# Kernel optimization log

Measured on AMD Instinct MI355X. Metric: run time of the kernel, lower is better.

The kernel has to match this reference:

```python
import jax, jax.numpy as jnp
import numpy as np

XBOUND = (-30.0, 30.0, 0.25)
YBOUND = (-15.0, 15.0, 0.25)
ZBOUND = (-1.0, 1.0, 0.5)
EPS = 1e-9


def _heights():
    n = int((ZBOUND[1] - ZBOUND[0]) // ZBOUND[2]) + 1
    return [ZBOUND[0] + i * ZBOUND[2] for i in range(n)]


def _bev_planes():
    # matches construct_plane_grid: linspace endpoints included, meshgrid(y, x) 'ij'
    num_x = int((XBOUND[1] - XBOUND[0]) / XBOUND[2])
    num_y = int((YBOUND[1] - YBOUND[0]) / YBOUND[2])
    x = jnp.linspace(XBOUND[0], XBOUND[1], num_x, dtype=jnp.float32)
    y = jnp.linspace(YBOUND[0], YBOUND[1], num_y, dtype=jnp.float32)
    yy, xx = jnp.meshgrid(y, x, indexing='ij')
    planes = [jnp.stack([xx, yy, jnp.full_like(xx, h)], axis=-1) for h in _heights()]
    return jnp.stack(planes)  # (nlvl, bH, bW, 3)


def _bilinear_grid_sample(im, grid):
    # faithful port of the manual pad+floor+gather grid_sample (align_corners=False)
    n, c, h, w = im.shape
    gh, gw = grid.shape[1], grid.shape[2]
    x = ((grid[..., 0] + 1) * w - 1) / 2
    y = ((grid[..., 1] + 1) * h - 1) / 2
    x = x.reshape(n, -1)
    y = y.reshape(n, -1)
    x0 = jnp.floor(x)
    y0 = jnp.floor(y)
    wa = ((x0 + 1 - x) * (y0 + 1 - y))[:, None, :]
    wb = ((x0 + 1 - x) * (y - y0))[:, None, :]
    wc = ((x - x0) * (y0 + 1 - y))[:, None, :]
    wd = ((x - x0) * (y - y0))[:, None, :]
    pw, ph = w + 2, h + 2
    # clip in float first to avoid int32 overflow; out-of-range lands on zero padding either way
    x0f = jnp.clip(x0, -2.0, w + 2.0)
    y0f = jnp.clip(y0, -2.0, h + 2.0)
    x0i = jnp.clip(x0f.astype(jnp.int32) + 1, 0, pw - 1)
    x1i = jnp.clip(x0f.astype(jnp.int32) + 2, 0, pw - 1)
    y0i = jnp.clip(y0f.astype(jnp.int32) + 1, 0, ph - 1)
    y1i = jnp.clip(y0f.astype(jnp.int32) + 2, 0, ph - 1)
    im_flat = jnp.pad(im, ((0, 0), (0, 0), (1, 1), (1, 1))).reshape(n, c, -1)

    def gather(xi, yi):
        return jnp.take_along_axis(im_flat, (xi + yi * pw)[:, None, :], axis=2)

    out = (gather(x0i, y0i) * wa + gather(x0i, y1i) * wb
           + gather(x1i, y0i) * wc + gather(x1i, y1i) * wd)
    return out.reshape(n, c, gh, gw)


def _campos(pts, ego2cam, img_h, img_w):
    # pts: (B, q, 3); ego2cam: (B, ncam, 4, 4)
    B, q, _ = pts.shape
    ncam = ego2cam.shape[1]
    pts_h = jnp.concatenate([pts, jnp.ones_like(pts[..., :1])], axis=-1)  # (B,q,4)
    cam = jnp.einsum('bnij,bqj->bnqi', ego2cam, pts_h)  # (B,ncam,q,4)
    z = cam[..., 2:3]
    mask = z > EPS
    xy = cam[..., 0:2] / z + EPS
    px = xy[..., 0:1] / img_w
    py = xy[..., 1:2] / img_h
    p = (jnp.concatenate([px, py], axis=-1) - 0.5) * 2
    mask = (mask & (p[..., 0:1] > -1.0) & (p[..., 0:1] < 1.0)
            & (p[..., 1:2] > -1.0) & (p[..., 1:2] < 1.0))
    return p.reshape(B * ncam, q, 2), mask.reshape(B, ncam, q)


def reference(cam_feat, ego2cam, conv_w, conv_b, img_h, img_w):
    B, ncam = ego2cam.shape[0], ego2cam.shape[1]
    C = cam_feat.shape[1]
    planes = _bev_planes().astype(cam_feat.dtype)  # (nlvl,bH,bW,3)
    nlvl, bH, bW, _ = planes.shape
    pts = jnp.broadcast_to(planes.reshape(1, -1, 3), (B, nlvl * bH * bW, 3))
    pos, mask = _campos(pts, ego2cam, img_h, img_w)
    grid = pos.reshape(B * ncam, nlvl * bH, bW, 2)
    proj = _bilinear_grid_sample(cam_feat, grid).reshape(B, ncam, C, nlvl, bH, bW)
    m = mask.reshape(B, ncam, 1, nlvl, bH, bW).astype(proj.dtype)
    feat = (proj * m).sum(axis=1)            # (B,C,nlvl,bH,bW)
    num = m.sum(axis=1)                      # (B,1,nlvl,bH,bW)
    feat = feat / jnp.where(num == 0, jnp.ones_like(num), num)
    coords = jnp.broadcast_to(jnp.transpose(planes, (3, 0, 1, 2))[None], (B, 3, nlvl, bH, bW))
    feat = jnp.concatenate([feat, coords], axis=1).reshape(B, (C + 3) * nlvl, bH, bW)
    out = jax.lax.conv_general_dilated(
        feat, conv_w, window_strides=(1, 1), padding=((1, 1), (1, 1)),
        dimension_numbers=('NCHW', 'OIHW', 'NCHW'))
    return out + conv_b[None, :, None, None]


def setup_inputs() -> dict:
    key = jax.random.key(0)
    k1, k2, k3 = jax.random.split(key, 3)
    B, ncam, C = 1, 6, 128
    cH, cW = 64, 176
    nlvl = 5
    cam_feat = jax.random.normal(k1, (B * ncam, C, cH, cW), dtype=jnp.float32)
    ego2cam = jax.random.normal(k2, (B, ncam, 4, 4), dtype=jnp.float32)
    conv_w = jax.random.normal(k3, (128, (C + 3) * nlvl, 3, 3), dtype=jnp.float32) * 0.02
    conv_b = jnp.zeros((128,), dtype=jnp.float32)
    return {'cam_feat': cam_feat, 'ego2cam': ego2cam, 'conv_w': conv_w,
            'conv_b': conv_b, 'img_h': 512, 'img_w': 1408}
```

## Files before the change

### kernel.cpp

```cpp
#include <hip/hip_runtime.h>
#include <hip/hip_bf16.h>

#define BH 120
#define BW 240
#define NLVL 5
#define NCAM 6
#define CH 128
#define FH 64
#define FW 176
#define CIN 655
#define CINP 672
#define NCT 21
#define FROWS 124
#define FCOLS 242
#define NPIX (BH*BW)

typedef __hip_bfloat16 bf16;
typedef __attribute__((ext_vector_type(8))) short s16x8;
typedef __attribute__((ext_vector_type(4))) float f32x4;
typedef unsigned int uint;
typedef __attribute__((ext_vector_type(4), aligned(4))) uint uint4a;

#define G_AS __attribute__((address_space(1)))
#define L_AS __attribute__((address_space(3)))

__device__ __forceinline__ float bf2f(unsigned short u) {
    union { unsigned int i; float f; } c; c.i = ((unsigned int)u) << 16; return c.f;
}
__device__ __forceinline__ uint f2bu(float x) {
    return (uint)__hip_bfloat16_raw(__float2bfloat16(x)).x;
}
__device__ __forceinline__ float blo(uint u) {
    union { uint i; float f; } c; c.i = u << 16; return c.f;
}
__device__ __forceinline__ float bhi(uint u) {
    union { uint i; float f; } c; c.i = u & 0xFFFF0000u; return c.f;
}

__global__ __launch_bounds__(256) void transpose_kernel(
    const float* __restrict__ in, bf16* __restrict__ out)
{
    __shared__ float t[32][129];
    int n = blockIdx.z, h = blockIdx.y, w0 = blockIdx.x * 32;
    int wlim = min(32, FW - w0);
    int wx = threadIdx.x & 31, cg = threadIdx.x >> 5;
    if (wx < wlim) {
        #pragma unroll
        for (int k = 0; k < 16; ++k) {
            int c = cg + k * 8;
            t[wx][c] = in[((n*CH + c)*FH + h)*FW + w0 + wx];
        }
    }
    __syncthreads();
    int c2 = threadIdx.x & 127, wi = threadIdx.x >> 7;
    for (int w = wi; w < wlim; w += 2)
        out[((n*FH + h)*FW + w0 + w)*CH + c2] = __float2bfloat16(t[w][c2]);
}

__global__ __launch_bounds__(256) void wprep_kernel(
    const float* __restrict__ w, bf16* __restrict__ wbf)
{
    int idx = blockIdx.x * 256 + threadIdx.x;
    if (idx >= 128 * CINP) return;
    int oc = idx / CINP, cin = idx - oc * CINP;
    float v[9];
    if (cin < CIN) {
        const float* s = w + ((size_t)oc * CIN + cin) * 9;
        #pragma unroll
        for (int k = 0; k < 9; ++k) v[k] = s[k];
    } else {
        #pragma unroll
        for (int k = 0; k < 9; ++k) v[k] = 0.f;
    }
    #pragma unroll
    for (int k = 0; k < 9; ++k)
        wbf[(size_t)(k * 128 + oc) * CINP + cin] = __float2bfloat16(v[k]);
}

__global__ __launch_bounds__(128) void border_kernel(bf16* __restrict__ feat)
{
    int b = blockIdx.x;
    int row, col;
    if (b < 242)      { row = 0;   col = b; }
    else if (b < 484) { row = 121; col = b - 242; }
    else if (b < 604) { row = b - 484 + 1; col = 0; }
    else              { row = b - 604 + 1; col = 241; }
    s16x8* p = (s16x8*)(feat + ((size_t)row*FCOLS + col)*CINP);
    int t = threadIdx.x;
    if (t < 84) p[t] = (s16x8){0,0,0,0,0,0,0,0};
}

__global__ __launch_bounds__(256) void proj_kernel(
    const bf16* __restrict__ camt,
    const float* __restrict__ e2c,
    const int* __restrict__ pimgh, const int* __restrict__ pimgw,
    bf16* __restrict__ feat)
{
    __shared__ int   s_soff[4][32];
    __shared__ float s_w4[4][30][4];
    __shared__ int   s_val[4][32];

    const int wv = threadIdx.x >> 6;
    const int lane = threadIdx.x & 63;
    const int bid = blockIdx.x;
    const int swz = (bid & 7) * 900 + (bid >> 3);
    const int pix = swz * 4 + wv;
    const int bx = pix % BW, by = pix / BW;
    float xw = (float)(-30.0 + bx * (60.0/239.0)); if (bx == BW-1) xw = 30.f;
    float yw = (float)(-15.0 + by * (30.0/119.0)); if (by == BH-1) yw = 15.f;

    const bool act = lane < 30;
    int valid = 0, ix = 0, iy = 0, cam = 0;
    float fx = 0.f, fy = 0.f;
    if (act) {
        int l = lane / 6; cam = lane - l*6;
        float h = -1.f + 0.5f * (float)l;
        const float* M = e2c + cam * 16;
        float cx = M[0]*xw + M[1]*yw + M[2]*h  + M[3];
        float cy = M[4]*xw + M[5]*yw + M[6]*h  + M[7];
        float cz = M[8]*xw + M[9]*yw + M[10]*h + M[11];
        float iw = (float)pimgw[0], ih = (float)pimgh[0];
        float px = ((cx/cz + 1e-9f)/iw - 0.5f) * 2.f;
        float py = ((cy/cz + 1e-9f)/ih - 0.5f) * 2.f;
        valid = (cz > 1e-9f) && (px > -1.f) && (px < 1.f)
                             && (py > -1.f) && (py < 1.f);
        float xs = ((px + 1.f)*(float)FW - 1.f) * 0.5f;
        float ys = ((py + 1.f)*(float)FH - 1.f) * 0.5f;
        float x0 = floorf(xs), y0 = floorf(ys);
        fx = xs - x0; fy = ys - y0;
        ix = (int)x0; iy = (int)y0;
        s_val[wv][lane] = valid;
    }
    __syncthreads();
    if (act) {
        int lbase = (lane / 6) * 6;
        int cnt = s_val[wv][lbase] + s_val[wv][lbase+1] + s_val[wv][lbase+2]
                + s_val[wv][lbase+3] + s_val[wv][lbase+4] + s_val[wv][lbase+5];
        float inv = (cnt > 0) ? (1.f / (float)cnt) : 0.f;
        float sc = valid ? inv : 0.f;
        int bx0 = min(max(ix, 0), FW-2);
        int by0 = min(max(iy, 0), FH-2);
        float gx0 = (1.f - fx) * sc, gx1 = fx * sc;
        float wx0 = 0.f, wx1 = 0.f;
        if (ix >= 0)     { if (ix == bx0) wx0 += gx0; else wx1 += gx0; }
        if (ix+1 <= FW-1){ if (ix+1 == bx0) wx0 += gx1; else wx1 += gx1; }
        float wy0 = 0.f, wy1 = 0.f;
        float gy0 = 1.f - fy, gy1 = fy;
        if (iy >= 0)     { if (iy == by0) wy0 += gy0; else wy1 += gy0; }
        if (iy+1 <= FH-1){ if (iy+1 == by0) wy0 += gy1; else wy1 += gy1; }
        s_w4[wv][lane][0] = wx0 * wy0;
        s_w4[wv][lane][1] = wx0 * wy1;
        s_w4[wv][lane][2] = wx1 * wy0;
        s_w4[wv][lane][3] = wx1 * wy1;
        s_soff[wv][lane] = valid ? ((cam*FH + by0)*FW + bx0)*CH : -1;
    }
    __syncthreads();

    const int c2 = lane * 2;
    float va[NLVL], vb[NLVL];
    #pragma unroll
    for (int l = 0; l < NLVL; ++l) { va[l] = 0.f; vb[l] = 0.f; }

    #pragma unroll
    for (int l = 0; l < NLVL; ++l) {
        #pragma unroll
        for (int cm = 0; cm < NCAM; ++cm) {
            int id = l*6 + cm;
            int so = s_soff[wv][id];
            if (so >= 0) {
                const bf16* bp = camt + so + c2;
                uint q0 = *(const uint*)(bp);
                uint q2 = *(const uint*)(bp + CH);
                uint q1 = *(const uint*)(bp + FW*CH);
                uint q3 = *(const uint*)(bp + FW*CH + CH);
                float w0 = s_w4[wv][id][0], w1 = s_w4[wv][id][1];
                float w2 = s_w4[wv][id][2], w3 = s_w4[wv][id][3];
                va[l] += w0*blo(q0) + w1*blo(q1) + w2*blo(q2) + w3*blo(q3);
                vb[l] += w0*bhi(q0) + w1*bhi(q1) + w2*bhi(q2) + w3*bhi(q3);
            }
        }
    }

    bf16* dpix = feat + ((size_t)(by+1)*FCOLS + (bx+1))*CINP;
    uint u0 = f2bu(va[0]) | (f2bu(va[1]) << 16);
    uint u1 = f2bu(va[2]) | (f2bu(va[3]) << 16);
    uint u2 = f2bu(va[4]) | (f2bu(vb[0]) << 16);
    uint u3 = f2bu(vb[1]) | (f2bu(vb[2]) << 16);
    uint u4 = f2bu(vb[3]) | (f2bu(vb[4]) << 16);
    char* dst = (char*)(dpix + c2*5);
    *(uint4a*)dst = (uint4a){u0, u1, u2, u3};
    *(uint*)(dst + 16) = u4;
    if (lane < 15) {
        int j = lane / 5, l = lane - j*5;
        float v = (j == 0) ? xw : (j == 1) ? yw : (-1.f + 0.5f*(float)l);
        dpix[CH*5 + lane] = __float2bfloat16(v);
    }
}

__global__ __launch_bounds__(256, 2) void conv_mfma_kernel(
    const bf16* __restrict__ feat,
    const bf16* __restrict__ wbf,
    bf16* __restrict__ part)
{
    __shared__ __align__(16) char lds[61440];
    const int tid  = threadIdx.x;
    const int wv   = tid >> 6;
    const int lane = tid & 63;
    const int t15  = tid & 15;
    const int kgl  = (tid >> 4) & 3;
    const int y0p = blockIdx.y * 8;
    const int x0p = blockIdx.x * 32;
    const int q   = blockIdx.z;
    const int ct0 = q ? (1 + 5*q) : 0;
    const int nct = q ? 5 : 6;
    const int nph = nct * 9;

    const int HB0 = 0, HB1 = 22528, WB0 = 45056, WB1 = 53248;

    f32x4 acc[8][4];
    #pragma unroll
    for (int m = 0; m < 8; ++m)
        #pragma unroll
        for (int f = 0; f < 4; ++f)
            acc[m][f] = (f32x4){0.f, 0.f, 0.f, 0.f};

    auto stageW = [&](int ct, int off, int wb) {
        #pragma unroll
        for (int jj = 0; jj < 2; ++jj) {
            int j = 2*wv + jj;
            int cch = j*64 + lane;
            int oc = cch >> 2, kgp = cch & 3;
            int kg = kgp ^ ((oc >> 1) & 3);
            const bf16* src = wbf + ((size_t)(off*128 + oc)*CINP + ct*32 + kg*8);
            __builtin_amdgcn_global_load_lds((const G_AS void*)src,
                                             (L_AS void*)(lds + wb + j*1024),
                                             16, 0, 0);
        }
    };
    auto stageH = [&](int ct, int hb) {
        for (int j = wv; j < 22; j += 4) {
            int cch = j*64 + lane;
            int pp = cch >> 2, kgp = cch & 3;
            int kg = kgp ^ ((pp >> 1) & 3);
            int row = pp / 34;
            int col = pp - row*34;
            int gc = min(x0p + col, FCOLS-1);
            const bf16* src = feat + ((size_t)(y0p + row)*FCOLS + gc)*CINP
                                   + ct*32 + kg*8;
            __builtin_amdgcn_global_load_lds((const G_AS void*)src,
                                             (L_AS void*)(lds + hb + j*1024),
                                             16, 0, 0);
        }
    };

    stageH(ct0, HB0);
    stageW(ct0, 0, WB0);
    __syncthreads();

    int lct = 0, off = 0;
    for (int p = 0; p < nph; ++p) {
        if (p + 1 < nph) {
            int off1 = off + 1, lct1 = lct;
            if (off1 == 9) { off1 = 0; ++lct1; }
            stageW(ct0 + lct1, off1, ((p+1) & 1) ? WB1 : WB0);
            if (off1 == 0) stageH(ct0 + lct1, (lct1 & 1) ? HB1 : HB0);
        }
        const int wb = (p & 1) ? WB1 : WB0;
        const int hb = (lct & 1) ? HB1 : HB0;
        const int ky = off / 3, kx = off - ky*3;

        s16x8 A[8];
        #pragma unroll
        for (int m = 0; m < 8; ++m) {
            int oc = m*16 + t15;
            A[m] = *(const s16x8*)(lds + wb + oc*64 + ((kgl ^ ((oc>>1)&3)) << 4));
        }
        #pragma unroll
        for (int f = 0; f < 4; ++f) {
            const int fr = f >> 1, fc = f & 1;
            int hp = (2*wv + fr + ky)*34 + fc*16 + t15 + kx;
            s16x8 Bv = *(const s16x8*)(lds + hb + hp*64
                                       + ((kgl ^ ((hp>>1)&3)) << 4));
            __builtin_amdgcn_s_setprio(1);
            #pragma unroll
            for (int m = 0; m < 8; ++m)
                acc[m][f] = __builtin_amdgcn_mfma_f32_16x16x32_bf16(
                                A[m], Bv, acc[m][f], 0, 0, 0);
            __builtin_amdgcn_s_setprio(0);
        }
        __syncthreads();
        if (++off == 9) { off = 0; ++lct; }
    }

    bf16* pq = part + (size_t)q * (128*NPIX);
    #pragma unroll
    for (int f = 0; f < 4; ++f) {
        const int fr = f >> 1, fc = f & 1;
        const int x = x0p + fc*16 + t15;
        if (x < BW) {
            const int y = y0p + 2*wv + fr;
            #pragma unroll
            for (int m = 0; m < 8; ++m) {
                #pragma unroll
                for (int r = 0; r < 4; ++r) {
                    int oc = m*16 + kgl*4 + r;
                    pq[(size_t)oc*NPIX + y*BW + x] = __float2bfloat16(acc[m][f][r]);
                }
            }
        }
    }
}

__global__ __launch_bounds__(256) void combine_kernel(
    const bf16* __restrict__ part, const float* __restrict__ bias,
    float* __restrict__ out)
{
    int i8 = blockIdx.x * 256 + threadIdx.x;
    if (i8 >= 128*NPIX/8) return;
    int oc = i8 / (NPIX/8);
    float s[8];
    float b = bias[oc];
    #pragma unroll
    for (int k = 0; k < 8; ++k) s[k] = b;
    #pragma unroll
    for (int qq = 0; qq < 4; ++qq) {
        s16x8 v = *(const s16x8*)(part + (size_t)qq*(128*NPIX) + (size_t)i8*8);
        #pragma unroll
        for (int k = 0; k < 8; ++k) s[k] += bf2f((unsigned short)v[k]);
    }
    f32x4* o = (f32x4*)(out + (size_t)i8*8);
    o[0] = (f32x4){s[0], s[1], s[2], s[3]};
    o[1] = (f32x4){s[4], s[5], s[6], s[7]};
}

extern "C" void kernel_launch(void* const* d_in, const int* in_sizes, int n_in,
                              void* d_out, int out_size, void* d_ws, size_t ws_size,
                              hipStream_t stream)
{
    const float* cam_feat = (const float*)d_in[0];
    const float* ego2cam  = (const float*)d_in[1];
    const float* conv_w   = (const float*)d_in[2];
    const float* conv_b   = (const float*)d_in[3];
    const int*   img_h    = (const int*)d_in[4];
    const int*   img_w    = (const int*)d_in[5];
    float* out = (float*)d_out;

    bf16* camt = (bf16*)d_ws;
    bf16* feat = camt + (size_t)NCAM*CH*FH*FW;
    bf16* wbf  = feat + (size_t)FROWS*FCOLS*CINP;
    bf16* part = wbf  + (size_t)9*128*CINP;

    transpose_kernel<<<dim3(6, FH, NCAM), 256, 0, stream>>>(cam_feat, camt);
    wprep_kernel<<<(128*CINP + 255)/256, 256, 0, stream>>>(conv_w, wbf);
    border_kernel<<<724, 128, 0, stream>>>(feat);
    proj_kernel<<<NPIX/4, 256, 0, stream>>>(camt, ego2cam, img_h, img_w, feat);
    conv_mfma_kernel<<<dim3(8, 15, 4), 256, 0, stream>>>(feat, wbf, part);
    combine_kernel<<<(128*NPIX/8 + 255)/256, 256, 0, stream>>>(part, conv_b, out);
}
```

Measured before the change: 105.5 us.

## Triple-buffer conv weight tiles with counted vmcnt waits and single barrier

Moves the conv MFMA kernel from double-buffered weight staging with two __syncthreads per phase to a triple-buffered weight ring that prefetches two phases ahead. The feature halo tile is now issued mid-tile, at offset 2, instead of at the tile boundary. Each phase does one explicit s_waitcnt vmcnt(N) followed by a raw s_barrier, so global-to-LDS loads can stay in flight across iterations. This is meant to hide load latency and cut barrier stalls. In exchange LDS grows from 60KB to 72KB, which may limit occupancy at 2 blocks per CU, and the hand-counted vmcnt values have to match the exact number of issued loads.

```diff
diff --git a/kernel.cpp b/kernel.cpp
--- a/kernel.cpp
+++ b/kernel.cpp
@@ -202,7 +202,7 @@
     const bf16* __restrict__ wbf,
     bf16* __restrict__ part)
 {
-    __shared__ __align__(16) char lds[61440];
+    __shared__ __align__(16) char lds[73728];
     const int tid  = threadIdx.x;
     const int wv   = tid >> 6;
     const int lane = tid & 63;
@@ -215,7 +215,8 @@
     const int nct = q ? 5 : 6;
     const int nph = nct * 9;
 
-    const int HB0 = 0, HB1 = 22528, WB0 = 45056, WB1 = 53248;
+    const int HB0 = 0, HB1 = 24576;
+    const int WB0 = 49152, WB1 = 57344, WB2 = 65536;
 
     f32x4 acc[8][4];
     #pragma unroll
@@ -238,7 +239,9 @@
         }
     };
     auto stageH = [&](int ct, int hb) {
-        for (int j = wv; j < 22; j += 4) {
+        #pragma unroll
+        for (int k = 0; k < 6; ++k) {
+            int j = wv + 4*k;
             int cch = j*64 + lane;
             int pp = cch >> 2, kgp = cch & 3;
             int kg = kgp ^ ((pp >> 1) & 3);
@@ -255,17 +258,27 @@
 
     stageH(ct0, HB0);
     stageW(ct0, 0, WB0);
-    __syncthreads();
+    stageW(ct0, 1, WB1);
 
     int lct = 0, off = 0;
-    for (int p = 0; p < nph; ++p) {
-        if (p + 1 < nph) {
-            int off1 = off + 1, lct1 = lct;
-            if (off1 == 9) { off1 = 0; ++lct1; }
-            stageW(ct0 + lct1, off1, ((p+1) & 1) ? WB1 : WB0);
-            if (off1 == 0) stageH(ct0 + lct1, (lct1 & 1) ? HB1 : HB0);
-        }
-        const int wb = (p & 1) ? WB1 : WB0;
+    for (int g = 0; g < nph; ++g) {
+        const bool hI = (lct + 1 < nct) && (off == 3 || off == 4);
+        if (g == nph - 1)      { asm volatile("s_waitcnt vmcnt(0)" ::: "memory"); }
+        else if (hI)           { asm volatile("s_waitcnt vmcnt(8)" ::: "memory"); }
+        else                   { asm volatile("s_waitcnt vmcnt(2)" ::: "memory"); }
+        __builtin_amdgcn_s_barrier();
+        asm volatile("" ::: "memory");
+
+        int g2 = g + 2;
+        if (g2 < nph) {
+            int lct2 = g2 / 9, off2 = g2 - lct2*9;
+            int wb2 = (g2 % 3 == 0) ? WB0 : (g2 % 3 == 1) ? WB1 : WB2;
+            stageW(ct0 + lct2, off2, wb2);
+        }
+        if (off == 2 && lct + 1 < nct)
+            stageH(ct0 + lct + 1, (lct & 1) ? HB0 : HB1);
+
+        const int wb = (g % 3 == 0) ? WB0 : (g % 3 == 1) ? WB1 : WB2;
         const int hb = (lct & 1) ? HB1 : HB0;
         const int ky = off / 3, kx = off - ky*3;
 
@@ -288,7 +301,6 @@
                                 A[m], Bv, acc[m][f], 0, 0, 0);
             __builtin_amdgcn_s_setprio(0);
         }
-        __syncthreads();
         if (++off == 9) { off = 0; ++lct; }
     }
 
```

Result: no change. 106.3 us (+0.7%).
